# Performance work log

Hardware: AMD Instinct MI355X
Metric: run time of the kernel (lower is better)

Reference implementation:

```python
import jax, jax.numpy as jnp
import numpy as np

N_QUBITS = 14
N_LAYERS = 4
N_CLASSES = 10
BATCH = 1024


def apply_1q(state, gate, wire):
    """Apply a 2x2 gate ([2,2] shared or [B,2,2] batched) to `wire` of state [B,2,...,2]."""
    s = jnp.moveaxis(state, wire + 1, -1)
    shp = s.shape
    s = s.reshape(shp[0], -1, 2)
    if gate.ndim == 3:
        s = jnp.einsum('bij,bkj->bki', gate, s)
    else:
        s = jnp.einsum('ij,bkj->bki', gate, s)
    return jnp.moveaxis(s.reshape(shp), -1, wire + 1)


def apply_cnot(state, c, t):
    s = jnp.moveaxis(state, (c + 1, t + 1), (-2, -1))
    s = jnp.stack([s[..., 0, :], s[..., 1, ::-1]], axis=-2)
    return jnp.moveaxis(s, (-2, -1), (c + 1, t + 1))


def simulate(x, q_params):
    """Batched statevector sim of: RY(x_i) embed -> BasicEntanglerLayers(RX + CNOT ring) -> <Z_i>."""
    B, n = x.shape
    state = jnp.zeros((B,) + (2,) * n, jnp.complex64)
    state = state.at[(slice(None),) + (0,) * n].set(1.0)

    # RY(x_i) on each wire (angles batched per sample)
    c, s = jnp.cos(0.5 * x), jnp.sin(0.5 * x)
    for w in range(n):
        g = jnp.stack([jnp.stack([c[:, w], -s[:, w]], -1),
                       jnp.stack([s[:, w], c[:, w]], -1)], -2).astype(jnp.complex64)  # [B,2,2]
        state = apply_1q(state, g, w)

    # BasicEntanglerLayers: per layer RX(weights[l,i]) on every wire, then CNOT ring
    cw, sw = jnp.cos(0.5 * q_params), jnp.sin(0.5 * q_params)
    n_layers = q_params.shape[0]
    for l in range(n_layers):
        for w in range(n):
            cc = cw[l, w].astype(jnp.complex64)
            isw = (-1j) * sw[l, w].astype(jnp.complex64)
            g = jnp.stack([jnp.stack([cc, isw]), jnp.stack([isw, cc])])  # [2,2] RX
            state = apply_1q(state, g, w)
        if n == 2:
            state = apply_cnot(state, 0, 1)
        else:
            for w in range(n):
                state = apply_cnot(state, w, (w + 1) % n)

    # <Z_i> = P(bit_i=0) - P(bit_i=1)
    p = jnp.abs(state) ** 2  # [B,2,...,2] real
    axes_all = tuple(range(1, n + 1))
    z = []
    for w in range(n):
        pw = jnp.sum(p, axis=tuple(a for a in axes_all if a != w + 1))  # [B,2]
        z.append(pw[:, 0] - pw[:, 1])
    return jnp.stack(z, -1).astype(jnp.float32)  # [B, n]


def setup_inputs() -> dict:
    key = jax.random.key(0)
    k1, k2, k3, k4 = jax.random.split(key, 4)
    x = jax.random.normal(k1, (BATCH, N_QUBITS), dtype=jnp.float32)
    q_params = 0.01 * jax.random.normal(k2, (N_LAYERS, N_QUBITS), dtype=jnp.float32)
    fc_w = jax.random.normal(k3, (N_CLASSES, N_QUBITS), dtype=jnp.float32) / np.sqrt(N_QUBITS)
    fc_b = jax.random.normal(k4, (N_CLASSES,), dtype=jnp.float32) * 0.01
    return {"x": x, "q_params": q_params, "fc_w": fc_w, "fc_b": fc_b}


def reference(x, q_params, fc_w, fc_b):
    q_out = simulate(x, q_params)            # [B, n_qubits]
    logits = q_out @ fc_w.T + fc_b           # [B, n_classes]
    return logits
```

## Files before the change

kernel.cpp:

```cpp
#include <hip/hip_runtime.h>
#include <hip/hip_fp16.h>
#include <math.h>


#define NQ 14
#define NLAYERS 4
#define NCLASSES 10
#define BLOCK 512

typedef _Float16 f16;
typedef _Float16 f16x2 __attribute__((ext_vector_type(2)));
typedef _Float16 f16x8 __attribute__((ext_vector_type(8)));
typedef _Float16 f16x4 __attribute__((ext_vector_type(4)));
typedef float f32x4 __attribute__((ext_vector_type(4)));
typedef unsigned int u32;
typedef u32 u32x2 __attribute__((ext_vector_type(2)));

__device__ __forceinline__ f32x4 mf(f16x8 a, f16x8 b, f32x4 c) {
  return __builtin_amdgcn_mfma_f32_16x16x32_f16(a, b, c, 0, 0, 0);
}
__device__ __forceinline__ int swz(int t) { return ((t ^ (t >> 3)) & 7) << 3; }

__device__ __forceinline__ f16x4 cvt4(f32x4 v) {
  u32x2 r;
  r[0] = __builtin_bit_cast(u32, __builtin_amdgcn_cvt_pkrtz(v[0], v[1]));
  r[1] = __builtin_bit_cast(u32, __builtin_amdgcn_cvt_pkrtz(v[2], v[3]));
  return __builtin_bit_cast(f16x4, r);
}

__device__ __forceinline__ int finv5(int n) {
  n ^= ((n >> 3) & 1) << 4;
  n ^= ((n >> 2) & 1) << 3;
  n ^= ((n >> 1) & 1) << 2;
  n ^= (n & 1) << 1;
  return n;
}
__device__ __forceinline__ int finv3(int n) {
  n ^= ((n >> 2) & 1) << 3;
  n ^= ((n >> 1) & 1) << 2;
  n ^= (n & 1) << 1;
  return n;
}

__device__ __forceinline__ void build32(f16* Bc, const float* qc, const float* qs,
                                        int base, int tid) {
  const float c0 = qc[base], c1 = qc[base+1], c2 = qc[base+2], c3 = qc[base+3], c4 = qc[base+4];
  const float s0 = qs[base], s1 = qs[base+1], s2 = qs[base+2], s3 = qs[base+3], s4 = qs[base+4];
#pragma unroll
  for (int e = tid; e < 1024; e += BLOCK) {
    const int n = e >> 5, k = e & 31;
    const int d = finv5(n) ^ k;
    float mag = ((d & 1) ? s0 : c0) * ((d & 2) ? s1 : c1);
    mag *= ((d & 4) ? s2 : c2) * ((d & 8) ? s3 : c3);
    mag *= ((d & 16) ? s4 : c4);
    const int t = __popc(d) & 3;
    const f16 v = (f16)((t == 1 || t == 2) ? -mag : mag);
    const int p = 256 * (k >> 3) + 8 * n + (k & 7);
    const bool isreal = !(t & 1);
    Bc[p]        = isreal ? v : (f16)0.f;
    Bc[p + 1024] = isreal ? (f16)0.f : v;
  }
}
__device__ __forceinline__ void buildC(f16* Bc, const float* qc, const float* qs,
                                       int base, int tid) {
  const float c0 = qc[base], c1 = qc[base+1], c2 = qc[base+2], c3 = qc[base+3];
  const float s0 = qs[base], s1 = qs[base+1], s2 = qs[base+2], s3 = qs[base+3];
  const int n = tid >> 5, k = tid & 31;
  f16 vr = (f16)0.f, vi = (f16)0.f;
  if (k < 16) {
    const int d = finv3(n) ^ k;
    float mag = ((d & 1) ? s0 : c0) * ((d & 2) ? s1 : c1);
    mag *= ((d & 4) ? s2 : c2) * ((d & 8) ? s3 : c3);
    const int t = __popc(d) & 3;
    const f16 v = (f16)((t == 1 || t == 2) ? -mag : mag);
    if (t & 1) vi = v; else vr = v;
  }
  const int p = 256 * (k >> 3) + 8 * n + (k & 7);
  Bc[p]        = vr;
  Bc[p + 1024] = vi;
}

template<bool CTRL, bool STORE_C>
__device__ __forceinline__ void pass32(f16* __restrict__ reP, f16* __restrict__ imP,
                                       const f16* __restrict__ BcR, int tid) {
  const int lane = tid & 63, wave = tid >> 6;
  const int q = lane >> 4, cc = lane & 15;
  int n0 = cc, n1 = cc | 16;
  if (CTRL && wave >= 4) { n0 ^= 31; n1 ^= 31; }
  const f16x8 br0 = *(const f16x8*)(BcR + 256 * q + 8 * n0);
  const f16x8 bi0 = *(const f16x8*)(BcR + 1024 + 256 * q + 8 * n0);
  const f16x8 br1 = *(const f16x8*)(BcR + 256 * q + 8 * n1);
  const f16x8 bi1 = *(const f16x8*)(BcR + 1024 + 256 * q + 8 * n1);
  f16x4 outR[8], outI[8];
#pragma unroll
  for (int i = 0; i < 4; ++i) {
    const int mt = wave * 4 + i;
    const int pA = mt * 512 + ((128 * q + 8 * cc) ^ swz(mt));
    const f16x8 Ar = *(const f16x8*)(reP + pA);
    const f16x8 Ai = *(const f16x8*)(imP + pA);
    const f16x8 nAi = -Ai;
    {
      f32x4 aR = {0.f,0.f,0.f,0.f}, aI = {0.f,0.f,0.f,0.f};
      aR = mf(Ar, br0, aR); aR = mf(nAi, bi0, aR);
      aI = mf(Ar, bi0, aI); aI = mf(Ai, br0, aI);
      outR[i * 2 + 0] = cvt4(aR);
      outI[i * 2 + 0] = cvt4(aI);
    }
    {
      f32x4 aR = {0.f,0.f,0.f,0.f}, aI = {0.f,0.f,0.f,0.f};
      aR = mf(Ar, br1, aR); aR = mf(nAi, bi1, aR);
      aI = mf(Ar, bi1, aI); aI = mf(Ai, br1, aI);
      outR[i * 2 + 1] = cvt4(aR);
      outI[i * 2 + 1] = cvt4(aI);
    }
  }
  __syncthreads();
#pragma unroll
  for (int i = 0; i < 4; ++i) {
    const int mt = wave * 4 + i;
#pragma unroll
    for (int nt = 0; nt < 2; ++nt) {
      const int n5 = nt * 16 + cc;
      int pS;
      if constexpr (STORE_C) {
        const int tC = (mt >> 4) + 2 * n5;
        pS = tC * 256 + ((128 * (q >> 1) + 8 * (mt & 15) + 4 * (q & 1)) ^ swz(tC));
      } else {
        pS = n5 * 512 + ((128 * (2 * (mt & 1) + (q >> 1)) + 8 * (mt >> 1) + 4 * (q & 1)) ^ swz(n5));
      }
      *(f16x4*)(reP + pS) = outR[i * 2 + nt];
      *(f16x4*)(imP + pS) = outI[i * 2 + nt];
    }
  }
}

template<bool FINAL>
__device__ __forceinline__ void passC(f16* __restrict__ reP, f16* __restrict__ imP,
                                      const f16* __restrict__ BcR, int tid,
                                      float* __restrict__ zloc) {
  const int lane = tid & 63, wave = tid >> 6;
  const int q = lane >> 4, cc = lane & 15;
  int n0 = cc;
  if (wave >= 4) n0 ^= 15;
  const f16x8 br = *(const f16x8*)(BcR + 256 * q + 8 * n0);
  const f16x8 bi = *(const f16x8*)(BcR + 1024 + 256 * q + 8 * n0);
  f16x4 outR[8], outI[8];
#pragma unroll
  for (int i = 0; i < 8; ++i) {
    const int mtC = wave * 8 + i;
    const int pA = mtC * 256 + ((128 * (q & 1) + 8 * cc) ^ swz(mtC));
    const f16x8 Ar = *(const f16x8*)(reP + pA);
    const f16x8 Ai = *(const f16x8*)(imP + pA);
    const f16x8 nAi = -Ai;
    f32x4 aR = {0.f,0.f,0.f,0.f}, aI = {0.f,0.f,0.f,0.f};
    aR = mf(Ar, br, aR); aR = mf(nAi, bi, aR);
    aI = mf(Ar, bi, aI); aI = mf(Ai, br, aI);
    if constexpr (FINAL) {
      float p0 = aR[0]*aR[0] + aI[0]*aI[0];
      float p1 = aR[1]*aR[1] + aI[1]*aI[1];
      float p2 = aR[2]*aR[2] + aI[2]*aI[2];
      float p3 = aR[3]*aR[3] + aI[3]*aI[3];
      if (cc & 8) { float t = p0; p0 = p1; p1 = t; t = p2; p2 = p3; p3 = t; }
      const float ps = p0 + p1 + p2 + p3;
      zloc[0] += (p0 - p1) + (p2 - p3);
      zloc[1] += (p0 + p1) - (p2 + p3);
      zloc[2] += (q & 1) ? -ps : ps;
      zloc[3] += (q & 2) ? -ps : ps;
#pragma unroll
      for (int w = 0; w < 6; ++w) zloc[4 + w] += ((mtC >> w) & 1) ? -ps : ps;
#pragma unroll
      for (int w = 0; w < 4; ++w) zloc[10 + w] += ((cc >> w) & 1) ? -ps : ps;
    } else {
      if (cc & 8) {
        f32x4 tR = aR, tI = aI;
        aR[0] = tR[1]; aR[1] = tR[0]; aR[2] = tR[3]; aR[3] = tR[2];
        aI[0] = tI[1]; aI[1] = tI[0]; aI[2] = tI[3]; aI[3] = tI[2];
      }
      outR[i] = cvt4(aR);
      outI[i] = cvt4(aI);
    }
  }
  if constexpr (!FINAL) {
    __syncthreads();
#pragma unroll
    for (int i = 0; i < 8; ++i) {
      const int mtC = wave * 8 + i;
      const int tP = 2 * cc + (mtC >> 5);
      const int pS = tP * 512 +
          ((128 * (2 * (mtC & 1) + (q >> 1)) + 8 * ((mtC >> 1) & 15) + 4 * (q & 1)) ^ swz(tP));
      *(f16x4*)(reP + pS) = outR[i];
      *(f16x4*)(imP + pS) = outI[i];
    }
  }
}

__global__ __launch_bounds__(BLOCK, 4) void qsim_kernel(
    const float* __restrict__ x, const float* __restrict__ qp,
    const float* __restrict__ fcw, const float* __restrict__ fcb,
    float* __restrict__ out) {
  extern __shared__ unsigned char smem[];
  f16* reP = (f16*)smem;
  f16* imP = reP + 16384;
  f16* Bc  = imP + 16384;
  float* qc = (float*)(Bc + 2048);
  float* qs = qc + 56;
  float* xc = qs + 56;
  float* xs = xc + 14;

  const int b = blockIdx.x;
  const int tid = threadIdx.x;

  if (tid < NQ) {
    float sv, cv; sincosf(0.5f * x[b * NQ + tid], &sv, &cv);
    xc[tid] = cv; xs[tid] = sv;
  } else if (tid >= 64 && tid < 64 + NLAYERS * NQ) {
    const int k = tid - 64;
    float sv, cv; sincosf(0.5f * qp[k], &sv, &cv);
    qc[k] = cv; qs[k] = sv;
  }
  __syncthreads();

  float* Flo  = (float*)Bc;
  float* psi  = Flo + 32;
  float* PsiR = psi + 32;
  float* PsiI = PsiR + 32;
  if (tid < 32) {
    float f = 1.f;
#pragma unroll
    for (int j = 0; j < 5; ++j) f *= ((tid >> j) & 1) ? xs[5 + j] : xc[5 + j];
    Flo[tid] = f;
  } else if (tid < 64) {
    const int k = tid - 32;
    float f = 1.f;
#pragma unroll
    for (int j = 0; j < 5; ++j) f *= ((k >> j) & 1) ? xs[j] : xc[j];
    psi[k] = f;
  }
  __syncthreads();
  if (tid < 32) {
    const float c0 = qc[0], c1 = qc[1], c2 = qc[2], c3 = qc[3], c4 = qc[4];
    const float s0 = qs[0], s1 = qs[1], s2 = qs[2], s3 = qs[3], s4 = qs[4];
    const int a = finv5(tid);
    float ar = 0.f, ai = 0.f;
    for (int k = 0; k < 32; ++k) {
      const int d = a ^ k;
      float mag = ((d & 1) ? s0 : c0) * ((d & 2) ? s1 : c1);
      mag *= ((d & 4) ? s2 : c2) * ((d & 8) ? s3 : c3);
      mag *= ((d & 16) ? s4 : c4);
      mag *= psi[k];
      const int t = __popc(d) & 3;
      if (t == 0) ar += mag; else if (t == 1) ai -= mag;
      else if (t == 2) ar -= mag; else ai += mag;
    }
    PsiR[tid] = ar; PsiI[tid] = ai;
  }
  __syncthreads();
  {
    float fhi = 1.f;
#pragma unroll
    for (int j = 0; j < 4; ++j) fhi *= ((tid >> j) & 1) ? xs[10 + j] : xc[10 + j];
    const float cr = fhi * PsiR[tid >> 4], ci = fhi * PsiI[tid >> 4];
    const int t = tid >> 4;
    const int sz = swz(t);
    float Fl[32];
#pragma unroll
    for (int j = 0; j < 32; ++j) Fl[j] = Flo[j];
    __syncthreads();
#pragma unroll
    for (int kb = 0; kb < 4; ++kb) {
      f16x8 hr, hi;
#pragma unroll
      for (int j = 0; j < 8; ++j) {
        const float F = Fl[8 * kb + j];
        hr[j] = (f16)(F * cr);
        hi[j] = (f16)(F * ci);
      }
      const int pb = t * 512 + ((128 * kb + 8 * (tid & 15)) ^ sz);
      *(f16x8*)(reP + pb) = hr;
      *(f16x8*)(imP + pb) = hi;
    }
  }
  build32(Bc, qc, qs, 0 * NQ + 5, tid);
  __syncthreads();

  pass32<true, true>(reP, imP, Bc, tid);          __syncthreads();
  buildC(Bc, qc, qs, 0 * NQ + 10, tid);           __syncthreads();
  passC<false>(reP, imP, Bc, tid, nullptr);       __syncthreads();
#pragma unroll
  for (int l = 1; l < NLAYERS; ++l) {
    build32(Bc, qc, qs, l * NQ + 0, tid);         __syncthreads();
    pass32<false, false>(reP, imP, Bc, tid);      __syncthreads();
    build32(Bc, qc, qs, l * NQ + 5, tid);         __syncthreads();
    pass32<true, true>(reP, imP, Bc, tid);        __syncthreads();
    buildC(Bc, qc, qs, l * NQ + 10, tid);         __syncthreads();
    if (l < NLAYERS - 1) {
      passC<false>(reP, imP, Bc, tid, nullptr);   __syncthreads();
    }
  }

  float zloc[NQ];
#pragma unroll
  for (int w = 0; w < NQ; ++w) zloc[w] = 0.f;
  passC<true>(reP, imP, Bc, tid, zloc);
  __syncthreads();

  float* zpart = (float*)Bc;
  float* zbuf  = zpart + 112;
#pragma unroll
  for (int w = 0; w < NQ; ++w) {
#pragma unroll
    for (int off = 32; off > 0; off >>= 1)
      zloc[w] += __shfl_down(zloc[w], off, 64);
  }
  const int wave = tid >> 6, lane = tid & 63;
  if (lane == 0) {
#pragma unroll
    for (int w = 0; w < NQ; ++w) zpart[wave * NQ + w] = zloc[w];
  }
  __syncthreads();
  if (tid < NQ) {
    float a = 0.f;
#pragma unroll
    for (int v = 0; v < 8; ++v) a += zpart[v * NQ + tid];
    zbuf[tid] = a;
  }
  __syncthreads();
  if (tid < NCLASSES) {
    float acc = fcb[tid];
#pragma unroll
    for (int w = 0; w < NQ; ++w) acc = fmaf(zbuf[w], fcw[tid * NQ + w], acc);
    out[b * NCLASSES + tid] = acc;
  }
}

extern "C" void kernel_launch(void* const* d_in, const int* in_sizes, int n_in,
                              void* d_out, int out_size, void* d_ws, size_t ws_size,
                              hipStream_t stream) {
  const float* x   = (const float*)d_in[0];
  const float* qp  = (const float*)d_in[1];
  const float* fcw = (const float*)d_in[2];
  const float* fcb = (const float*)d_in[3];
  float* out = (float*)d_out;
  const int B = in_sizes[0] / NQ;

  const size_t shmem = (size_t)(2 * 16384 + 2048) * sizeof(f16)
                     + (size_t)(56 + 56 + 14 + 14) * sizeof(float);
  (void)hipFuncSetAttribute((const void*)qsim_kernel,
                            hipFuncAttributeMaxDynamicSharedMemorySize, (int)shmem);
  qsim_kernel<<<B, BLOCK, shmem, stream>>>(x, qp, fcw, fcb, out);
}
```

Before: 140.9 us.

## Fuse 32-wide and 16-wide gate passes into one register-resident pass

Merges the second 5-qubit pass and the final 4-qubit pass of each layer into one routine. The 32-wide MFMA result is converted to fp16 and fed straight into a 16x16x16 MFMA against a small 16x16 gate matrix held in registers, which removes one full shared-memory round-trip of the state and two barriers per layer. The C-gate matrix is built in its own buffer alongside the B matrix, and outputs are repacked with byte permutes into the layout the next pass expects. The expectation-value reduction is rewritten for the new register layout, which adds complexity in bit-to-wire mapping and an extra fp16 rounding between the two fused stages.

```diff
diff --git a/kernel.cpp b/kernel.cpp
--- a/kernel.cpp
+++ b/kernel.cpp
@@ -10,14 +10,17 @@
 
 typedef _Float16 f16;
 typedef _Float16 f16x2 __attribute__((ext_vector_type(2)));
+typedef _Float16 f16x4 __attribute__((ext_vector_type(4)));
 typedef _Float16 f16x8 __attribute__((ext_vector_type(8)));
-typedef _Float16 f16x4 __attribute__((ext_vector_type(4)));
 typedef float f32x4 __attribute__((ext_vector_type(4)));
 typedef unsigned int u32;
 typedef u32 u32x2 __attribute__((ext_vector_type(2)));
 
 __device__ __forceinline__ f32x4 mf(f16x8 a, f16x8 b, f32x4 c) {
   return __builtin_amdgcn_mfma_f32_16x16x32_f16(a, b, c, 0, 0, 0);
+}
+__device__ __forceinline__ f32x4 mf16(f16x4 a, f16x4 b, f32x4 c) {
+  return __builtin_amdgcn_mfma_f32_16x16x16f16(a, b, c, 0, 0, 0);
 }
 __device__ __forceinline__ int swz(int t) { return ((t ^ (t >> 3)) & 7) << 3; }
 
@@ -26,6 +29,9 @@
   r[0] = __builtin_bit_cast(u32, __builtin_amdgcn_cvt_pkrtz(v[0], v[1]));
   r[1] = __builtin_bit_cast(u32, __builtin_amdgcn_cvt_pkrtz(v[2], v[3]));
   return __builtin_bit_cast(f16x4, r);
+}
+__device__ __forceinline__ u32 dwof(f16x4 v, int k) {
+  return __builtin_bit_cast(u32x2, v)[k];
 }
 
 __device__ __forceinline__ int finv5(int n) {
@@ -61,32 +67,31 @@
     Bc[p + 1024] = isreal ? (f16)0.f : v;
   }
 }
-__device__ __forceinline__ void buildC(f16* Bc, const float* qc, const float* qs,
-                                       int base, int tid) {
-  const float c0 = qc[base], c1 = qc[base+1], c2 = qc[base+2], c3 = qc[base+3];
-  const float s0 = qs[base], s1 = qs[base+1], s2 = qs[base+2], s3 = qs[base+3];
-  const int n = tid >> 5, k = tid & 31;
-  f16 vr = (f16)0.f, vi = (f16)0.f;
-  if (k < 16) {
-    const int d = finv3(n) ^ k;
+
+__device__ __forceinline__ void buildC2(f16* Cc, const float* qc, const float* qs,
+                                        int base, int tid) {
+  if (tid < 256) {
+    const float c0 = qc[base], c1 = qc[base+1], c2 = qc[base+2], c3 = qc[base+3];
+    const float s0 = qs[base], s1 = qs[base+1], s2 = qs[base+2], s3 = qs[base+3];
+    const int rp = tid >> 4, k = tid & 15;
+    const int d = finv3(rp) ^ k;
     float mag = ((d & 1) ? s0 : c0) * ((d & 2) ? s1 : c1);
     mag *= ((d & 4) ? s2 : c2) * ((d & 8) ? s3 : c3);
     const int t = __popc(d) & 3;
     const f16 v = (f16)((t == 1 || t == 2) ? -mag : mag);
-    if (t & 1) vi = v; else vr = v;
-  }
-  const int p = 256 * (k >> 3) + 8 * n + (k & 7);
-  Bc[p]        = vr;
-  Bc[p + 1024] = vi;
-}
-
-template<bool CTRL, bool STORE_C>
-__device__ __forceinline__ void pass32(f16* __restrict__ reP, f16* __restrict__ imP,
-                                       const f16* __restrict__ BcR, int tid) {
+    const bool isreal = !(t & 1);
+    const int p = 16 * rp + k;
+    Cc[p]       = isreal ? v : (f16)0.f;
+    Cc[p + 256] = isreal ? (f16)0.f : v;
+    Cc[p + 512] = isreal ? (f16)0.f : (f16)(-v);
+  }
+}
+
+__device__ __forceinline__ void passA(f16* __restrict__ reP, f16* __restrict__ imP,
+                                      const f16* __restrict__ BcR, int tid) {
   const int lane = tid & 63, wave = tid >> 6;
   const int q = lane >> 4, cc = lane & 15;
-  int n0 = cc, n1 = cc | 16;
-  if (CTRL && wave >= 4) { n0 ^= 31; n1 ^= 31; }
+  const int n0 = cc, n1 = cc | 16;
   const f16x8 br0 = *(const f16x8*)(BcR + 256 * q + 8 * n0);
   const f16x8 bi0 = *(const f16x8*)(BcR + 1024 + 256 * q + 8 * n0);
   const f16x8 br1 = *(const f16x8*)(BcR + 256 * q + 8 * n1);
@@ -121,13 +126,8 @@
 #pragma unroll
     for (int nt = 0; nt < 2; ++nt) {
       const int n5 = nt * 16 + cc;
-      int pS;
-      if constexpr (STORE_C) {
-        const int tC = (mt >> 4) + 2 * n5;
-        pS = tC * 256 + ((128 * (q >> 1) + 8 * (mt & 15) + 4 * (q & 1)) ^ swz(tC));
-      } else {
-        pS = n5 * 512 + ((128 * (2 * (mt & 1) + (q >> 1)) + 8 * (mt >> 1) + 4 * (q & 1)) ^ swz(n5));
-      }
+      const int pS = n5 * 512 +
+          ((128 * (2 * (mt & 1) + (q >> 1)) + 8 * (mt >> 1) + 4 * (q & 1)) ^ swz(n5));
       *(f16x4*)(reP + pS) = outR[i * 2 + nt];
       *(f16x4*)(imP + pS) = outI[i * 2 + nt];
     }
@@ -135,61 +135,103 @@
 }
 
 template<bool FINAL>
-__device__ __forceinline__ void passC(f16* __restrict__ reP, f16* __restrict__ imP,
-                                      const f16* __restrict__ BcR, int tid,
-                                      float* __restrict__ zloc) {
+__device__ __forceinline__ void superBC(f16* __restrict__ reP, f16* __restrict__ imP,
+                                        const f16* __restrict__ BcR,
+                                        const f16* __restrict__ Cc,
+                                        int tid, float* __restrict__ zloc) {
   const int lane = tid & 63, wave = tid >> 6;
   const int q = lane >> 4, cc = lane & 15;
-  int n0 = cc;
-  if (wave >= 4) n0 ^= 15;
-  const f16x8 br = *(const f16x8*)(BcR + 256 * q + 8 * n0);
-  const f16x8 bi = *(const f16x8*)(BcR + 1024 + 256 * q + 8 * n0);
-  f16x4 outR[8], outI[8];
-#pragma unroll
-  for (int i = 0; i < 8; ++i) {
-    const int mtC = wave * 8 + i;
-    const int pA = mtC * 256 + ((128 * (q & 1) + 8 * cc) ^ swz(mtC));
+  int n0 = cc, n1 = cc | 16;
+  if (wave >= 4) { n0 ^= 31; n1 ^= 31; }
+  const f16x8 br0 = *(const f16x8*)(BcR + 256 * q + 8 * n0);
+  const f16x8 bi0 = *(const f16x8*)(BcR + 1024 + 256 * q + 8 * n0);
+  const f16x8 br1 = *(const f16x8*)(BcR + 256 * q + 8 * n1);
+  const f16x8 bi1 = *(const f16x8*)(BcR + 1024 + 256 * q + 8 * n1);
+  const int r0 = 16 * cc + 4 * q, r1 = 16 * (cc ^ 15) + 4 * q;
+  const f16x4 ucr0 = *(const f16x4*)(Cc + r0);
+  const f16x4 uci0 = *(const f16x4*)(Cc + 256 + r0);
+  const f16x4 ucn0 = *(const f16x4*)(Cc + 512 + r0);
+  const f16x4 ucr1 = *(const f16x4*)(Cc + r1);
+  const f16x4 uci1 = *(const f16x4*)(Cc + 256 + r1);
+  const f16x4 ucn1 = *(const f16x4*)(Cc + 512 + r1);
+
+  f16x4 accR[4][2], accI[4][2];
+  float z0b = 0.f, z1b = 0.f, z9b = 0.f, zA = 0.f, zB = 0.f, pt = 0.f;
+#pragma unroll
+  for (int i = 0; i < 4; ++i) {
+    const int mt = wave * 4 + i;
+    const int pA = mt * 512 + ((128 * q + 8 * cc) ^ swz(mt));
     const f16x8 Ar = *(const f16x8*)(reP + pA);
     const f16x8 Ai = *(const f16x8*)(imP + pA);
     const f16x8 nAi = -Ai;
-    f32x4 aR = {0.f,0.f,0.f,0.f}, aI = {0.f,0.f,0.f,0.f};
-    aR = mf(Ar, br, aR); aR = mf(nAi, bi, aR);
-    aI = mf(Ar, bi, aI); aI = mf(Ai, br, aI);
-    if constexpr (FINAL) {
-      float p0 = aR[0]*aR[0] + aI[0]*aI[0];
-      float p1 = aR[1]*aR[1] + aI[1]*aI[1];
-      float p2 = aR[2]*aR[2] + aI[2]*aI[2];
-      float p3 = aR[3]*aR[3] + aI[3]*aI[3];
-      if (cc & 8) { float t = p0; p0 = p1; p1 = t; t = p2; p2 = p3; p3 = t; }
-      const float ps = p0 + p1 + p2 + p3;
-      zloc[0] += (p0 - p1) + (p2 - p3);
-      zloc[1] += (p0 + p1) - (p2 + p3);
-      zloc[2] += (q & 1) ? -ps : ps;
-      zloc[3] += (q & 2) ? -ps : ps;
-#pragma unroll
-      for (int w = 0; w < 6; ++w) zloc[4 + w] += ((mtC >> w) & 1) ? -ps : ps;
-#pragma unroll
-      for (int w = 0; w < 4; ++w) zloc[10 + w] += ((cc >> w) & 1) ? -ps : ps;
-    } else {
-      if (cc & 8) {
-        f32x4 tR = aR, tI = aI;
-        aR[0] = tR[1]; aR[1] = tR[0]; aR[2] = tR[3]; aR[3] = tR[2];
-        aI[0] = tI[1]; aI[1] = tI[0]; aI[2] = tI[3]; aI[3] = tI[2];
+#pragma unroll
+    for (int h = 0; h < 2; ++h) {
+      const f16x8 br = h ? br1 : br0;
+      const f16x8 bi = h ? bi1 : bi0;
+      f32x4 aR = {0.f,0.f,0.f,0.f}, aI = {0.f,0.f,0.f,0.f};
+      aR = mf(Ar, br, aR); aR = mf(nAi, bi, aR);
+      aI = mf(Ar, bi, aI); aI = mf(Ai, br, aI);
+      const f16x4 s1r = cvt4(aR), s1i = cvt4(aI);
+      const f16x4 ur = h ? ucr1 : ucr0;
+      const f16x4 ui = h ? uci1 : uci0;
+      const f16x4 un = h ? ucn1 : ucn0;
+      f32x4 cR = {0.f,0.f,0.f,0.f}, cI = {0.f,0.f,0.f,0.f};
+      cR = mf16(ur, s1r, cR); cR = mf16(un, s1i, cR);
+      cI = mf16(ui, s1r, cI); cI = mf16(ur, s1i, cI);
+      if constexpr (FINAL) {
+        const float p0 = cR[0]*cR[0] + cI[0]*cI[0];
+        const float p1 = cR[1]*cR[1] + cI[1]*cI[1];
+        const float p2 = cR[2]*cR[2] + cI[2]*cI[2];
+        const float p3 = cR[3]*cR[3] + cI[3]*cI[3];
+        const float ps = (p0 + p1) + (p2 + p3);
+        zA += (p0 - p1) + (p2 - p3);
+        zB += (p0 + p1) - (p2 + p3);
+        z0b += (i & 1) ? -ps : ps;
+        z1b += (i & 2) ? -ps : ps;
+        z9b += h ? -ps : ps;
+        pt  += ps;
+      } else {
+        accR[i][h] = cvt4(cR);
+        accI[i][h] = cvt4(cI);
       }
-      outR[i] = cvt4(aR);
-      outI[i] = cvt4(aI);
-    }
-  }
-  if constexpr (!FINAL) {
+    }
+  }
+  if constexpr (FINAL) {
+    zloc[0]  += (q & 2) ? -z0b : z0b;
+    zloc[1]  += z1b;
+    zloc[2]  += (wave & 1) ? -pt : pt;
+    zloc[3]  += (wave & 2) ? -pt : pt;
+    zloc[4]  += (wave & 4) ? -pt : pt;
+    zloc[5]  += (cc & 1) ? -pt : pt;
+    zloc[6]  += (cc & 2) ? -pt : pt;
+    zloc[7]  += (cc & 4) ? -pt : pt;
+    zloc[8]  += (cc & 8) ? -pt : pt;
+    zloc[9]  += z9b;
+    zloc[10] += zA;
+    zloc[11] += zB;
+    zloc[12] += (q & 1) ? -pt : pt;
+    zloc[13] += (q & 2) ? -pt : pt;
+  } else {
     __syncthreads();
-#pragma unroll
-    for (int i = 0; i < 8; ++i) {
-      const int mtC = wave * 8 + i;
-      const int tP = 2 * cc + (mtC >> 5);
-      const int pS = tP * 512 +
-          ((128 * (2 * (mtC & 1) + (q >> 1)) + 8 * ((mtC >> 1) & 15) + 4 * (q & 1)) ^ swz(tP));
-      *(f16x4*)(reP + pS) = outR[i];
-      *(f16x4*)(imP + pS) = outI[i];
+    const u32 selLo = (q & 2) ? 0x01000504u : 0x05040100u;
+    const u32 selHi = (q & 2) ? 0x03020706u : 0x07060302u;
+    const int ibase = 128 * (wave >> 1) + 4 * (wave & 1);
+#pragma unroll
+    for (int h = 0; h < 2; ++h) {
+#pragma unroll
+      for (int j = 0; j < 4; ++j) {
+        const int pS = (8 * q + 2 * j + h) * 512 + ibase +
+                       8 * (cc ^ (2 * j + h) ^ q);
+        const int dj = j >> 1;
+        const u32 sel = (j & 1) ? selHi : selLo;
+        u32x2 vr, vi;
+        vr[0] = __builtin_amdgcn_perm(dwof(accR[1][h], dj), dwof(accR[0][h], dj), sel);
+        vr[1] = __builtin_amdgcn_perm(dwof(accR[3][h], dj), dwof(accR[2][h], dj), sel);
+        vi[0] = __builtin_amdgcn_perm(dwof(accI[1][h], dj), dwof(accI[0][h], dj), sel);
+        vi[1] = __builtin_amdgcn_perm(dwof(accI[3][h], dj), dwof(accI[2][h], dj), sel);
+        *(u32x2*)(reP + pS) = vr;
+        *(u32x2*)(imP + pS) = vi;
+      }
     }
   }
 }
@@ -202,7 +244,8 @@
   f16* reP = (f16*)smem;
   f16* imP = reP + 16384;
   f16* Bc  = imP + 16384;
-  float* qc = (float*)(Bc + 2048);
+  f16* Cc  = Bc + 2048;
+  float* qc = (float*)(Cc + 768);
   float* qs = qc + 56;
   float* xc = qs + 56;
   float* xs = xc + 14;
@@ -281,27 +324,26 @@
     }
   }
   build32(Bc, qc, qs, 0 * NQ + 5, tid);
-  __syncthreads();
-
-  pass32<true, true>(reP, imP, Bc, tid);          __syncthreads();
-  buildC(Bc, qc, qs, 0 * NQ + 10, tid);           __syncthreads();
-  passC<false>(reP, imP, Bc, tid, nullptr);       __syncthreads();
+  buildC2(Cc, qc, qs, 0 * NQ + 10, tid);
+  __syncthreads();
+
+  superBC<false>(reP, imP, Bc, Cc, tid, nullptr);   __syncthreads();
 #pragma unroll
   for (int l = 1; l < NLAYERS; ++l) {
-    build32(Bc, qc, qs, l * NQ + 0, tid);         __syncthreads();
-    pass32<false, false>(reP, imP, Bc, tid);      __syncthreads();
-    build32(Bc, qc, qs, l * NQ + 5, tid);         __syncthreads();
-    pass32<true, true>(reP, imP, Bc, tid);        __syncthreads();
-    buildC(Bc, qc, qs, l * NQ + 10, tid);         __syncthreads();
+    build32(Bc, qc, qs, l * NQ + 0, tid);           __syncthreads();
+    passA(reP, imP, Bc, tid);                       __syncthreads();
+    build32(Bc, qc, qs, l * NQ + 5, tid);
+    buildC2(Cc, qc, qs, l * NQ + 10, tid);
+    __syncthreads();
     if (l < NLAYERS - 1) {
-      passC<false>(reP, imP, Bc, tid, nullptr);   __syncthreads();
+      superBC<false>(reP, imP, Bc, Cc, tid, nullptr); __syncthreads();
     }
   }
 
   float zloc[NQ];
 #pragma unroll
   for (int w = 0; w < NQ; ++w) zloc[w] = 0.f;
-  passC<true>(reP, imP, Bc, tid, zloc);
+  superBC<true>(reP, imP, Bc, Cc, tid, zloc);
   __syncthreads();
 
   float* zpart = (float*)Bc;
@@ -343,7 +385,7 @@
   float* out = (float*)d_out;
   const int B = in_sizes[0] / NQ;
 
-  const size_t shmem = (size_t)(2 * 16384 + 2048) * sizeof(f16)
+  const size_t shmem = (size_t)(2 * 16384 + 2048 + 768) * sizeof(f16)
                      + (size_t)(56 + 56 + 14 + 14) * sizeof(float);
   (void)hipFuncSetAttribute((const void*)qsim_kernel,
                             hipFuncAttributeMaxDynamicSharedMemorySize, (int)shmem);
```

Result: faster. 122.8 us (-12.8%).
